# Optimization experiments

Hardware: AMD Instinct MI355X
Metric: run time of the kernel (lower is better)

Reference implementation:

```python
import jax, jax.numpy as jnp
import numpy as np

N_WIRES = 8
DIM = 2 ** N_WIRES  # 256


def _rx(theta):
    # theta: [] or [N] -> [2,2] or [N,2,2] complex64
    c = jnp.cos(theta / 2)
    s = jnp.sin(theta / 2)
    return jnp.stack([jnp.stack([c + 0j, -1j * s], -1),
                      jnp.stack([-1j * s, c + 0j], -1)], -2)


def _ry(theta):
    c = jnp.cos(theta / 2)
    s = jnp.sin(theta / 2)
    return jnp.stack([jnp.stack([c + 0j, -s + 0j], -1),
                      jnp.stack([s + 0j, c + 0j], -1)], -2)


def _rz(theta):
    e = jnp.exp(-1j * theta / 2)
    z = jnp.zeros_like(e)
    return jnp.stack([jnp.stack([e, z], -1),
                      jnp.stack([z, jnp.conj(e)], -1)], -2)


def _apply_1q(state, U, wire):
    # state: [N, DIM]; U: [2,2] (shared) or [N,2,2] (per-sample)
    s = state.reshape(-1, 2 ** wire, 2, 2 ** (N_WIRES - 1 - wire))
    if U.ndim == 2:
        s = jnp.einsum('ab,nxby->nxay', U, s)
    else:
        s = jnp.einsum('nab,nxby->nxay', U, s)
    return s.reshape(-1, DIM)


def _cnot(state, c, t):
    # wire 0 = most significant bit (PennyLane convention)
    s = state.reshape((-1,) + (2,) * N_WIRES)
    ax_c = 1 + c
    s0 = jnp.take(s, 0, axis=ax_c)
    s1 = jnp.take(s, 1, axis=ax_c)
    ax_t = 1 + t if t < c else t  # target axis after control axis removed
    s1 = jnp.flip(s1, axis=ax_t)
    s = jnp.stack([s0, s1], axis=ax_c)
    return s.reshape(-1, DIM)


def _z_signs():
    idx = np.arange(DIM)
    bits = (idx[:, None] >> (N_WIRES - 1 - np.arange(N_WIRES))[None, :]) & 1
    return jnp.asarray(1.0 - 2.0 * bits, dtype=jnp.float32)  # [DIM, 8]


def _circuit(x_flat, params):
    # x_flat: [N, 8] angles; params: [8, 3]
    n = x_flat.shape[0]
    state = jnp.zeros((n, DIM), dtype=jnp.complex64).at[:, 0].set(1.0)
    for i in range(N_WIRES):
        state = _apply_1q(state, _rx(x_flat[:, i]), i)
    for i in range(N_WIRES):
        state = _apply_1q(state, _ry(params[i, 0]), i)
        state = _apply_1q(state, _rz(params[i, 1]), i)
        state = _apply_1q(state, _rx(params[i, 2]), i)
    for i in range(N_WIRES - 1):
        state = _cnot(state, i, i + 1)
    state = _cnot(state, N_WIRES - 1, 0)
    probs = state.real ** 2 + state.imag ** 2  # [N, DIM]
    return probs @ _z_signs()  # [N, 8] PauliZ expvals


def setup_inputs() -> dict:
    key = jax.random.key(0)
    ks = jax.random.split(key, 4)
    B, S = 16, 2048
    embed_dim, ffn_dim = 512, 2048
    return {
        'x': jax.random.normal(ks[0], (B, S, N_WIRES), dtype=jnp.float32),
        'params': jax.random.normal(ks[1], (N_WIRES, 3), dtype=jnp.float32),
        'W1': jax.random.normal(ks[2], (ffn_dim, N_WIRES), dtype=jnp.float32) * 0.1,
        'b1': jnp.zeros((ffn_dim,), dtype=jnp.float32),
        'W2': jax.random.normal(ks[3], (embed_dim, ffn_dim), dtype=jnp.float32) * 0.02,
        'b2': jnp.zeros((embed_dim,), dtype=jnp.float32),
    }


def reference(x, params, W1, b1, W2, b2):
    B, S, _ = x.shape
    ev = _circuit(x.reshape(-1, N_WIRES), params).reshape(B, S, N_WIRES)
    h = jax.nn.relu(ev @ W1.T + b1)
    return h @ W2.T + b2
```

## Files before the change

### kernel.cpp

```cpp
#include <hip/hip_runtime.h>
#include <hip/hip_bf16.h>

#define NS 32768
#define EMB 512
#define KDIM 2048

typedef float f32x16 __attribute__((ext_vector_type(16)));
typedef __bf16 bf16x8 __attribute__((ext_vector_type(8)));
typedef __bf16 bf16x2 __attribute__((ext_vector_type(2)));
typedef unsigned int u32;
typedef const __attribute__((address_space(1))) u32* gptr_t;
typedef __attribute__((address_space(3))) u32* lptr_t;

#if __has_builtin(__builtin_amdgcn_fdot2_f32_bf16)
#define HAS_FDOT2 1
#else
#define HAS_FDOT2 0
#endif

__device__ __forceinline__ void gload_lds16(const void* g, void* l) {
    __builtin_amdgcn_global_load_lds((gptr_t)g, (lptr_t)l, 16, 0, 0);
}

__global__ __launch_bounds__(256) void k_prep(const float* __restrict__ W2,
                                              const float* __restrict__ W1,
                                              __hip_bfloat16* __restrict__ W2b,
                                              __hip_bfloat16* __restrict__ W1bg) {
    int t = threadIdx.x;
    if (blockIdx.x < 1024) {
        int i = (blockIdx.x * 256 + t) * 4;
        float4 v = *(const float4*)(W2 + i);
        __hip_bfloat16 o[4];
        o[0] = __float2bfloat16(v.x); o[1] = __float2bfloat16(v.y);
        o[2] = __float2bfloat16(v.z); o[3] = __float2bfloat16(v.w);
        *(ulong1*)(W2b + i) = *(ulong1*)o;
    } else {
        int j = (blockIdx.x - 1024) * 1024 + t * 4;
        float4 w = *(const float4*)(W1 + j);
        __hip_bfloat16 p[4];
        p[0] = __float2bfloat16(w.x); p[1] = __float2bfloat16(w.y);
        p[2] = __float2bfloat16(w.z); p[3] = __float2bfloat16(w.w);
        *(ulong1*)(W1bg + j) = *(ulong1*)p;
    }
}

#define BM 128
#define BN 256

__global__ __launch_bounds__(256, 2) void k_gemm(
        const float* __restrict__ x,
        const float* __restrict__ params,
        const __hip_bfloat16* __restrict__ W1bg,
        const float* __restrict__ b1,
        const __hip_bfloat16* __restrict__ W2b,
        const float* __restrict__ b2,
        float* __restrict__ C) {
    __shared__ __hip_bfloat16 Bs[16 * 512];
    __shared__ __hip_bfloat16 W1s[KDIM * 8];
    __shared__ float b1s[KDIM];
    __shared__ __hip_bfloat16 evs[BM * 8];

    int tid = threadIdx.x, wave = tid >> 6, lane = tid & 63;
    int l31 = lane & 31, half = lane >> 5;
    int bx = blockIdx.x, bm = bx >> 1, bn = bx & 1;

    if (tid < 128) {
        float K1[8], K2[8];
        #pragma unroll
        for (int i = 0; i < 8; i++) {
            float a = params[i*3+0], b = params[i*3+1], g = params[i*3+2];
            float sa, ca, sb, cb, sg, cg;
            __sincosf(a, &sa, &ca);
            __sincosf(b, &sb, &cb);
            __sincosf(g, &sg, &cg);
            K1[i] = sa*sb*sg + ca*cg;
            K2[i] = cb*sg;
        }
        int n = bm * BM + tid;
        float4 x0 = *(const float4*)(x + (size_t)n*8);
        float4 x1 = *(const float4*)(x + (size_t)n*8 + 4);
        float xs[8] = {x0.x, x0.y, x0.z, x0.w, x1.x, x1.y, x1.z, x1.w};
        float z[8];
        #pragma unroll
        for (int i = 0; i < 8; i++) {
            float s, c;
            __sincosf(xs[i], &s, &c);
            z[i] = c * K1[i] - s * K2[i];
        }
        float evv[8];
        float p = z[0];
        #pragma unroll
        for (int j = 1; j < 8; j++) { p *= z[j]; evv[j] = p; }
        float sfx = z[7];
        #pragma unroll
        for (int j = 6; j >= 1; j--) sfx *= z[j];
        evv[0] = sfx;
        __hip_bfloat16 o[8];
        #pragma unroll
        for (int i = 0; i < 8; i++) o[i] = __float2bfloat16(evv[i]);
        *(bf16x8*)&evs[tid * 8] = *(bf16x8*)o;
    }
    for (int i = tid; i < KDIM; i += 256) {
        *(bf16x8*)&W1s[i * 8] = *(const bf16x8*)(W1bg + (size_t)i * 8);
        b1s[i] = b1[i];
    }
    __syncthreads();

    bf16x8 evr = *(const bf16x8*)&evs[(wave * 32 + l31) * 8];
#if HAS_FDOT2
    bf16x2 ep[4];
    #pragma unroll
    for (int p = 0; p < 4; p++) ep[p] = (bf16x2){evr[2*p], evr[2*p+1]};
#else
    float ef[8];
    #pragma unroll
    for (int i = 0; i < 8; i++) ef[i] = (float)evr[i];
#endif

    const __hip_bfloat16* gBp[4];
    #pragma unroll
    for (int i = 0; i < 4; i++) {
        int f = wave * 4 + i, ni = f >> 1, t = f & 1;
        gBp[i] = W2b + (size_t)(bn*BN + ni*32 + l31) * KDIM + t*16 + half*8;
    }

    f32x16 acc[8] = {};

    for (int k0 = 0; k0 < KDIM; k0 += 32) {
        #pragma unroll
        for (int i = 0; i < 4; i++) {
            gload_lds16(gBp[i], &Bs[(wave*4 + i) * 512]);
            gBp[i] += 32;
        }
        __syncthreads();

        #pragma unroll
        for (int t = 0; t < 2; t++) {
            int kb = k0 + t*16 + half*8;
            float4 ba = *(const float4*)&b1s[kb];
            float4 bb = *(const float4*)&b1s[kb + 4];
            float bv[8] = {ba.x, ba.y, ba.z, ba.w, bb.x, bb.y, bb.z, bb.w};
            bf16x8 af;
            #pragma unroll
            for (int j = 0; j < 8; j++) {
                bf16x8 w = *(const bf16x8*)&W1s[(kb + j) * 8];
                float a = bv[j];
#if HAS_FDOT2
                #pragma unroll
                for (int p = 0; p < 4; p++) {
                    bf16x2 wp = (bf16x2){w[2*p], w[2*p+1]};
                    a = __builtin_amdgcn_fdot2_f32_bf16(ep[p], wp, a, false);
                }
#else
                #pragma unroll
                for (int i = 0; i < 8; i++) a = fmaf(ef[i], (float)w[i], a);
#endif
                af[j] = (__bf16)fmaxf(a, 0.f);
            }
            #pragma unroll
            for (int ni = 0; ni < 8; ni++) {
                bf16x8 bfr = *(const bf16x8*)&Bs[(ni*2 + t) * 512 + lane * 8];
                acc[ni] = __builtin_amdgcn_mfma_f32_32x32x16_bf16(
                              af, bfr, acc[ni], 0, 0, 0);
            }
        }
        __syncthreads();
    }

    int rbase = bm*BM + wave*32 + 4*half;
    #pragma unroll
    for (int ni = 0; ni < 8; ni++) {
        int col = bn*BN + ni*32 + l31;
        float bias = b2[col];
        #pragma unroll
        for (int r = 0; r < 16; r++) {
            int row = rbase + (r & 3) + 8 * (r >> 2);
            C[(size_t)row * EMB + col] = acc[ni][r] + bias;
        }
    }
}

extern "C" void kernel_launch(void* const* d_in, const int* in_sizes, int n_in,
                              void* d_out, int out_size, void* d_ws, size_t ws_size,
                              hipStream_t stream) {
    const float* x      = (const float*)d_in[0];
    const float* params = (const float*)d_in[1];
    const float* W1     = (const float*)d_in[2];
    const float* b1     = (const float*)d_in[3];
    const float* W2     = (const float*)d_in[4];
    const float* b2     = (const float*)d_in[5];
    float* out = (float*)d_out;

    char* ws = (char*)d_ws;
    __hip_bfloat16* W2b  = (__hip_bfloat16*)ws;
    __hip_bfloat16* W1bg = (__hip_bfloat16*)(ws + 2097152);

    k_prep<<<1040, 256, 0, stream>>>(W2, W1, W2b, W1bg);
    k_gemm<<<(NS/BM) * (EMB/BN), 256, 0, stream>>>(x, params, W1bg, b1, W2b, b2, out);
}
```

Baseline: 177.6 us.

## Compute hidden activations with MFMA and share via double-buffered LDS

```diff
diff --git a/kernel.cpp b/kernel.cpp
--- a/kernel.cpp
+++ b/kernel.cpp
@@ -7,16 +7,10 @@
 
 typedef float f32x16 __attribute__((ext_vector_type(16)));
 typedef __bf16 bf16x8 __attribute__((ext_vector_type(8)));
-typedef __bf16 bf16x2 __attribute__((ext_vector_type(2)));
+typedef __bf16 bf16x4 __attribute__((ext_vector_type(4)));
 typedef unsigned int u32;
 typedef const __attribute__((address_space(1))) u32* gptr_t;
 typedef __attribute__((address_space(3))) u32* lptr_t;
-
-#if __has_builtin(__builtin_amdgcn_fdot2_f32_bf16)
-#define HAS_FDOT2 1
-#else
-#define HAS_FDOT2 0
-#endif
 
 __device__ __forceinline__ void gload_lds16(const void* g, void* l) {
     __builtin_amdgcn_global_load_lds((gptr_t)g, (lptr_t)l, 16, 0, 0);
@@ -24,8 +18,10 @@
 
 __global__ __launch_bounds__(256) void k_prep(const float* __restrict__ W2,
                                               const float* __restrict__ W1,
+                                              const float* __restrict__ b1,
                                               __hip_bfloat16* __restrict__ W2b,
-                                              __hip_bfloat16* __restrict__ W1bg) {
+                                              __hip_bfloat16* __restrict__ W1b,
+                                              __hip_bfloat16* __restrict__ b1b) {
     int t = threadIdx.x;
     if (blockIdx.x < 1024) {
         int i = (blockIdx.x * 256 + t) * 4;
@@ -35,12 +31,21 @@
         o[2] = __float2bfloat16(v.z); o[3] = __float2bfloat16(v.w);
         *(ulong1*)(W2b + i) = *(ulong1*)o;
     } else {
-        int j = (blockIdx.x - 1024) * 1024 + t * 4;
-        float4 w = *(const float4*)(W1 + j);
-        __hip_bfloat16 p[4];
-        p[0] = __float2bfloat16(w.x); p[1] = __float2bfloat16(w.y);
-        p[2] = __float2bfloat16(w.z); p[3] = __float2bfloat16(w.w);
-        *(ulong1*)(W1bg + j) = *(ulong1*)p;
+        __hip_bfloat16 bb[8];
+        #pragma unroll
+        for (int r = 0; r < 8; r++) {
+            int row = t * 8 + r;
+            float4 a = *(const float4*)(W1 + (size_t)row * 8);
+            float4 b = *(const float4*)(W1 + (size_t)row * 8 + 4);
+            __hip_bfloat16 p[8];
+            p[0] = __float2bfloat16(a.x); p[1] = __float2bfloat16(a.y);
+            p[2] = __float2bfloat16(a.z); p[3] = __float2bfloat16(a.w);
+            p[4] = __float2bfloat16(b.x); p[5] = __float2bfloat16(b.y);
+            p[6] = __float2bfloat16(b.z); p[7] = __float2bfloat16(b.w);
+            *(bf16x8*)(W1b + (size_t)row * 8) = *(bf16x8*)p;
+            bb[r] = __float2bfloat16(b1[row]);
+        }
+        *(bf16x8*)(b1b + t * 8) = *(bf16x8*)bb;
     }
 }
 
@@ -50,21 +55,28 @@
 __global__ __launch_bounds__(256, 2) void k_gemm(
         const float* __restrict__ x,
         const float* __restrict__ params,
-        const __hip_bfloat16* __restrict__ W1bg,
-        const float* __restrict__ b1,
+        const __hip_bfloat16* __restrict__ W1b,
+        const __hip_bfloat16* __restrict__ b1b,
         const __hip_bfloat16* __restrict__ W2b,
         const float* __restrict__ b2,
         float* __restrict__ C) {
-    __shared__ __hip_bfloat16 Bs[16 * 512];
     __shared__ __hip_bfloat16 W1s[KDIM * 8];
-    __shared__ float b1s[KDIM];
-    __shared__ __hip_bfloat16 evs[BM * 8];
+    __shared__ __hip_bfloat16 b1s[KDIM];
+    __shared__ __hip_bfloat16 hs[2][8][512];
 
     int tid = threadIdx.x, wave = tid >> 6, lane = tid & 63;
-    int l31 = lane & 31, half = lane >> 5;
+    int l31 = lane & 31, hh = lane >> 5;
+    int wr = wave >> 1, wc = wave & 1;
     int bx = blockIdx.x, bm = bx >> 1, bn = bx & 1;
 
-    if (tid < 128) {
+    #pragma unroll
+    for (int r = 0; r < 8; r++)
+        gload_lds16(W1b + (size_t)(r * 256 + tid) * 8, &W1s[(r * 256 + tid) * 8]);
+    gload_lds16(b1b + tid * 8, &b1s[tid * 8]);
+
+    int row = bm * BM + wave * 32 + l31;
+    float evv[8];
+    {
         float K1[8], K2[8];
         #pragma unroll
         for (int i = 0; i < 8; i++) {
@@ -76,9 +88,8 @@
             K1[i] = sa*sb*sg + ca*cg;
             K2[i] = cb*sg;
         }
-        int n = bm * BM + tid;
-        float4 x0 = *(const float4*)(x + (size_t)n*8);
-        float4 x1 = *(const float4*)(x + (size_t)n*8 + 4);
+        float4 x0 = *(const float4*)(x + (size_t)row * 8);
+        float4 x1 = *(const float4*)(x + (size_t)row * 8 + 4);
         float xs[8] = {x0.x, x0.y, x0.z, x0.w, x1.x, x1.y, x1.z, x1.w};
         float z[8];
         #pragma unroll
@@ -87,7 +98,6 @@
             __sincosf(xs[i], &s, &c);
             z[i] = c * K1[i] - s * K2[i];
         }
-        float evv[8];
         float p = z[0];
         #pragma unroll
         for (int j = 1; j < 8; j++) { p *= z[j]; evv[j] = p; }
@@ -95,87 +105,71 @@
         #pragma unroll
         for (int j = 6; j >= 1; j--) sfx *= z[j];
         evv[0] = sfx;
-        __hip_bfloat16 o[8];
-        #pragma unroll
-        for (int i = 0; i < 8; i++) o[i] = __float2bfloat16(evv[i]);
-        *(bf16x8*)&evs[tid * 8] = *(bf16x8*)o;
     }
-    for (int i = tid; i < KDIM; i += 256) {
-        *(bf16x8*)&W1s[i * 8] = *(const bf16x8*)(W1bg + (size_t)i * 8);
-        b1s[i] = b1[i];
-    }
+    bf16x8 evB;
+    #pragma unroll
+    for (int i = 0; i < 8; i++)
+        evB[i] = hh ? (__bf16)(i == 0 ? 1.f : 0.f) : (__bf16)evv[i];
+
     __syncthreads();
 
-    bf16x8 evr = *(const bf16x8*)&evs[(wave * 32 + l31) * 8];
-#if HAS_FDOT2
-    bf16x2 ep[4];
-    #pragma unroll
-    for (int p = 0; p < 4; p++) ep[p] = (bf16x2){evr[2*p], evr[2*p+1]};
-#else
-    float ef[8];
-    #pragma unroll
-    for (int i = 0; i < 8; i++) ef[i] = (float)evr[i];
-#endif
+    const __hip_bfloat16* Bbase = W2b + (size_t)(bn*BN + wc*128 + l31) * KDIM + hh * 8;
 
-    const __hip_bfloat16* gBp[4];
-    #pragma unroll
-    for (int i = 0; i < 4; i++) {
-        int f = wave * 4 + i, ni = f >> 1, t = f & 1;
-        gBp[i] = W2b + (size_t)(bn*BN + ni*32 + l31) * KDIM + t*16 + half*8;
+    f32x16 acc[2][4] = {};
+
+    #pragma unroll 2
+    for (int k0 = 0; k0 < KDIM; k0 += 32) {
+        int cb = (k0 >> 5) & 1;
+        bf16x8 Bf[8];
+        #pragma unroll
+        for (int ni = 0; ni < 4; ni++)
+            #pragma unroll
+            for (int t = 0; t < 2; t++)
+                Bf[ni*2+t] = *(const bf16x8*)(Bbase + (size_t)ni*32*KDIM + k0 + t*16);
+
+        bf16x8 w8 = *(const bf16x8*)&W1s[(k0 + l31) * 8];
+        __bf16 bias1 = ((const __bf16*)b1s)[k0 + l31];
+        bf16x8 aop;
+        #pragma unroll
+        for (int i = 0; i < 8; i++)
+            aop[i] = hh ? (i == 0 ? bias1 : (__bf16)0.f) : w8[i];
+        f32x16 ha = __builtin_amdgcn_mfma_f32_32x32x16_bf16(aop, evB, (f32x16){0}, 0, 0, 0);
+
+        #pragma unroll
+        for (int g = 0; g < 4; g++) {
+            bf16x4 hv;
+            #pragma unroll
+            for (int i = 0; i < 4; i++) hv[i] = (__bf16)fmaxf(ha[g*4+i], 0.f);
+            int slab = (g >> 1) * 4 + wave;
+            *(bf16x4*)&hs[cb][slab][(g & 1) * 256 + l31 * 8 + hh * 4] = hv;
+        }
+
+        asm volatile("s_waitcnt lgkmcnt(0)\n\ts_barrier" ::: "memory");
+
+        #pragma unroll
+        for (int t = 0; t < 2; t++)
+            #pragma unroll
+            for (int mi = 0; mi < 2; mi++) {
+                bf16x8 af = *(const bf16x8*)&hs[cb][t*4 + wr*2 + mi][hh * 256 + l31 * 8];
+                #pragma unroll
+                for (int ni = 0; ni < 4; ni++)
+                    acc[mi][ni] = __builtin_amdgcn_mfma_f32_32x32x16_bf16(
+                                      af, Bf[ni*2+t], acc[mi][ni], 0, 0, 0);
+            }
     }
 
-    f32x16 acc[8] = {};
-
-    for (int k0 = 0; k0 < KDIM; k0 += 32) {
+    #pragma unroll
+    for (int ni = 0; ni < 4; ni++) {
+        int col = bn*BN + wc*128 + ni*32 + l31;
+        float bias2 = b2[col];
         #pragma unroll
-        for (int i = 0; i < 4; i++) {
-            gload_lds16(gBp[i], &Bs[(wave*4 + i) * 512]);
-            gBp[i] += 32;
-        }
-        __syncthreads();
-
-        #pragma unroll
-        for (int t = 0; t < 2; t++) {
-            int kb = k0 + t*16 + half*8;
-            float4 ba = *(const float4*)&b1s[kb];
-            float4 bb = *(const float4*)&b1s[kb + 4];
-            float bv[8] = {ba.x, ba.y, ba.z, ba.w, bb.x, bb.y, bb.z, bb.w};
-            bf16x8 af;
+        for (int mi = 0; mi < 2; mi++) {
+            int rbase = bm*BM + wr*64 + mi*32 + 4*hh;
             #pragma unroll
-            for (int j = 0; j < 8; j++) {
-                bf16x8 w = *(const bf16x8*)&W1s[(kb + j) * 8];
-                float a = bv[j];
-#if HAS_FDOT2
-                #pragma unroll
-                for (int p = 0; p < 4; p++) {
-                    bf16x2 wp = (bf16x2){w[2*p], w[2*p+1]};
-                    a = __builtin_amdgcn_fdot2_f32_bf16(ep[p], wp, a, false);
-                }
-#else
-                #pragma unroll
-                for (int i = 0; i < 8; i++) a = fmaf(ef[i], (float)w[i], a);
-#endif
-                af[j] = (__bf16)fmaxf(a, 0.f);
+            for (int r = 0; r < 16; r++) {
+                int rr = rbase + (r & 3) + 8 * (r >> 2);
+                C[(size_t)rr * EMB + col] = acc[mi][ni][r] + bias2;
             }
-            #pragma unroll
-            for (int ni = 0; ni < 8; ni++) {
-                bf16x8 bfr = *(const bf16x8*)&Bs[(ni*2 + t) * 512 + lane * 8];
-                acc[ni] = __builtin_amdgcn_mfma_f32_32x32x16_bf16(
-                              af, bfr, acc[ni], 0, 0, 0);
-            }
-        }
-        __syncthreads();
-    }
-
-    int rbase = bm*BM + wave*32 + 4*half;
-    #pragma unroll
-    for (int ni = 0; ni < 8; ni++) {
-        int col = bn*BN + ni*32 + l31;
-        float bias = b2[col];
-        #pragma unroll
-        for (int r = 0; r < 16; r++) {
-            int row = rbase + (r & 3) + 8 * (r >> 2);
-            C[(size_t)row * EMB + col] = acc[ni][r] + bias;
         }
     }
 }
@@ -192,9 +186,10 @@
     float* out = (float*)d_out;
 
     char* ws = (char*)d_ws;
-    __hip_bfloat16* W2b  = (__hip_bfloat16*)ws;
-    __hip_bfloat16* W1bg = (__hip_bfloat16*)(ws + 2097152);
+    __hip_bfloat16* W2b = (__hip_bfloat16*)ws;
+    __hip_bfloat16* W1b = (__hip_bfloat16*)(ws + 2097152);
+    __hip_bfloat16* b1b = (__hip_bfloat16*)(ws + 2097152 + 32768);
 
-    k_prep<<<1040, 256, 0, stream>>>(W2, W1, W2b, W1bg);
-    k_gemm<<<(NS/BM) * (EMB/BN), 256, 0, stream>>>(x, params, W1bg, b1, W2b, b2, out);
+    k_prep<<<1025, 256, 0, stream>>>(W2, W1, b1, W2b, W1b, b1b);
+    k_gemm<<<(NS/BM) * (EMB/BN), 256, 0, stream>>>(x, params, W1b, b1b, W2b, b2, out);
 }
```

Result: slower. 204.9 us (+15.4%).
